# Kernel optimization log

Measured on AMD Instinct MI355X. Metric: run time of the kernel, lower is better.

Reference implementation:

```python
import jax, jax.numpy as jnp
import numpy as np
import math

DIM = 1024
N_HEADS = 16
HEAD_DIM = DIM // N_HEADS  # 64
B, S = 2, 2048


def apply_rope(x, cos, sin):
    # x: [b, s, h, d]; cos/sin: [s, d//2]
    xr = x[..., 0::2]
    xi = x[..., 1::2]
    cos = cos[None, :, None, :]
    sin = sin[None, :, None, :]
    out_r = xr * cos - xi * sin
    out_i = xr * sin + xi * cos
    # interleave back: stack pairs on last axis then flatten
    return jnp.stack([out_r, out_i], axis=-1).reshape(x.shape)


def setup_inputs() -> dict:
    key = jax.random.key(0)
    ks = jax.random.split(key, 8)
    scale = 1.0 / math.sqrt(DIM)
    x = jax.random.normal(ks[0], (B, S, DIM), dtype=jnp.float32)
    attn_mask = jnp.zeros((1, 1, S, S), dtype=jnp.float32)
    pos = jnp.arange(S, dtype=jnp.float32)[:, None]
    inv_freq = 1.0 / (10000.0 ** (jnp.arange(0, HEAD_DIM, 2, dtype=jnp.float32) / HEAD_DIM))
    ang = pos * inv_freq[None, :]  # [S, HEAD_DIM//2]
    freqs_cos = jnp.cos(ang)
    freqs_sin = jnp.sin(ang)
    wq_w = jax.random.normal(ks[1], (DIM, DIM), dtype=jnp.float32) * scale
    wk_w = jax.random.normal(ks[2], (DIM, DIM), dtype=jnp.float32) * scale
    wv_w = jax.random.normal(ks[3], (DIM, DIM), dtype=jnp.float32) * scale
    wo_w = jax.random.normal(ks[4], (DIM, DIM), dtype=jnp.float32) * scale
    wq_b = jnp.zeros((DIM,), dtype=jnp.float32)
    wk_b = jnp.zeros((DIM,), dtype=jnp.float32)
    wv_b = jnp.zeros((DIM,), dtype=jnp.float32)
    return {"x": x, "attn_mask": attn_mask, "freqs_cos": freqs_cos,
            "freqs_sin": freqs_sin, "wq_w": wq_w, "wq_b": wq_b,
            "wk_w": wk_w, "wk_b": wk_b, "wv_w": wv_w, "wv_b": wv_b,
            "wo_w": wo_w}


def reference(x, attn_mask, freqs_cos, freqs_sin, wq_w, wq_b, wk_w, wk_b,
              wv_w, wv_b, wo_w):
    b, s, _ = x.shape
    xq = (x @ wq_w + wq_b).reshape(b, s, N_HEADS, HEAD_DIM)
    xk = (x @ wk_w + wk_b).reshape(b, s, N_HEADS, HEAD_DIM)
    xv = (x @ wv_w + wv_b).reshape(b, s, N_HEADS, HEAD_DIM)
    xq = apply_rope(xq, freqs_cos, freqs_sin)
    xk = apply_rope(xk, freqs_cos, freqs_sin)
    # scores: [b, h, sq, skv]
    scores = jnp.einsum('bqhd,bkhd->bhqk', xq, xk) / math.sqrt(HEAD_DIM)
    scores = scores + attn_mask
    probs = jax.nn.softmax(scores, axis=-1)
    out = jnp.einsum('bhqk,bkhd->bqhd', probs, xv).reshape(b, s, DIM)
    return out @ wo_w
```

## Files before the change

### kernel.cpp

```cpp
#include <hip/hip_runtime.h>
#include <math.h>
#include <stdint.h>

#define DIM   1024
#define NH    16
#define HD    64
#define BATCH 2
#define SEQ   2048
#define ROWS  (BATCH*SEQ)

typedef __attribute__((ext_vector_type(8))) short short8;
typedef __attribute__((ext_vector_type(4))) float f32x4;

__device__ __forceinline__ unsigned short f2bf(float f) {
    union { float f; unsigned u; } x; x.f = f;
    unsigned r = x.u + 0x7FFFu + ((x.u >> 16) & 1u);
    return (unsigned short)(r >> 16);
}
__device__ __forceinline__ float bf2f(unsigned short h) {
    union { unsigned u; float f; } x; x.u = ((unsigned)h) << 16;
    return x.f;
}

#define MFMA(a,b,c) __builtin_amdgcn_mfma_f32_16x16x32_bf16((a),(b),(c),0,0,0)

__device__ __forceinline__ void gl_lds16(const void* g, void* l) {
    __builtin_amdgcn_global_load_lds(
        (const __attribute__((address_space(1))) unsigned int*)g,
        (__attribute__((address_space(3))) unsigned int*)l,
        16, 0, 0);
}

__global__ __launch_bounds__(256) void splitx_kernel(
    const float* __restrict__ x, unsigned short* __restrict__ xh, unsigned short* __restrict__ xl)
{
    const size_t i = ((size_t)blockIdx.x * 256 + threadIdx.x) * 4;
    const float4 v = *(const float4*)&x[i];
    ushort4 h, l;
    h.x = f2bf(v.x); l.x = f2bf(v.x - bf2f(h.x));
    h.y = f2bf(v.y); l.y = f2bf(v.y - bf2f(h.y));
    h.z = f2bf(v.z); l.z = f2bf(v.z - bf2f(h.z));
    h.w = f2bf(v.w); l.w = f2bf(v.w - bf2f(h.w));
    *(ushort4*)&xh[i] = h;
    *(ushort4*)&xl[i] = l;
}

__global__ __launch_bounds__(256) void splitw_kernel(
    const float* __restrict__ w0, const float* __restrict__ w1,
    const float* __restrict__ w2, const float* __restrict__ w3,
    unsigned short* __restrict__ wth, unsigned short* __restrict__ wtl)
{
    __shared__ float tile[64][68];
    const int z = blockIdx.z;
    const float* W = (z == 0) ? w0 : (z == 1) ? w1 : (z == 2) ? w2 : w3;
    unsigned short* th = wth + (size_t)z * DIM * DIM;
    unsigned short* tl = wtl + (size_t)z * DIM * DIM;
    const int k0 = blockIdx.y * 64, n0 = blockIdx.x * 64;
    const int tr = threadIdx.x >> 4, tc = (threadIdx.x & 15) * 4;
    #pragma unroll
    for (int p = 0; p < 4; ++p) {
        const float4 v = *(const float4*)&W[(size_t)(k0 + tr + p*16) * DIM + n0 + tc];
        *(float4*)&tile[tr + p*16][tc] = v;
    }
    __syncthreads();
    #pragma unroll
    for (int p = 0; p < 4; ++p) {
        const int n = tr + p*16;
        ushort4 hv, lv;
        float v0 = tile[tc+0][n], v1 = tile[tc+1][n], v2 = tile[tc+2][n], v3 = tile[tc+3][n];
        hv.x = f2bf(v0); lv.x = f2bf(v0 - bf2f(hv.x));
        hv.y = f2bf(v1); lv.y = f2bf(v1 - bf2f(hv.y));
        hv.z = f2bf(v2); lv.z = f2bf(v2 - bf2f(hv.z));
        hv.w = f2bf(v3); lv.w = f2bf(v3 - bf2f(hv.w));
        *(ushort4*)&th[(size_t)(n0 + n) * DIM + k0 + tc] = hv;
        *(ushort4*)&tl[(size_t)(n0 + n) * DIM + k0 + tc] = lv;
    }
}

template<int MODE>
__global__ __launch_bounds__(256, 2) void gemm3_kernel(
    const unsigned short* __restrict__ Ah, const unsigned short* __restrict__ Al,
    const unsigned short* __restrict__ Wh0, const unsigned short* __restrict__ Wl0,
    const unsigned short* __restrict__ Wh1, const unsigned short* __restrict__ Wl1,
    const unsigned short* __restrict__ Wh2, const unsigned short* __restrict__ Wl2,
    const float* __restrict__ b0, const float* __restrict__ b1, const float* __restrict__ b2,
    const float* __restrict__ fc, const float* __restrict__ fs,
    unsigned short* __restrict__ q_h, unsigned short* __restrict__ q_l,
    unsigned short* __restrict__ k_h, unsigned short* __restrict__ k_l,
    unsigned short* __restrict__ vt_h, unsigned short* __restrict__ vt_l,
    float* __restrict__ outf)
{
    __shared__ __align__(16) unsigned short lah[128*32], lal[128*32];
    __shared__ __align__(16) unsigned short lbh[128*32], lbl[128*32];

    const int tid = threadIdx.x;
    const int lane = tid & 63;
    const int lx = lane & 15, lg = lane >> 4;
    const int wv = tid >> 6, wm = wv >> 1, wn = wv & 1;
    const int n0 = blockIdx.x * 128, m0 = blockIdx.y * 128;
    const int z = (MODE == 0) ? blockIdx.z : 3;

    const unsigned short *Wh, *Wl;
    const float* bias;
    if (MODE == 0) {
        Wh = (z == 0) ? Wh0 : (z == 1) ? Wh1 : Wh2;
        Wl = (z == 0) ? Wl0 : (z == 1) ? Wl1 : Wl2;
        bias = (z == 0) ? b0 : (z == 1) ? b1 : b2;
    } else { Wh = Wh0; Wl = Wl0; bias = nullptr; }

    const int sr  = tid >> 2;
    const int scb = (tid & 3) << 4;

    f32x4 acc[4][4] = {};
    uint4 ra0, ra1, rl0, rl1, rb0, rb1, rb2, rb3;

    auto loadA = [&](int k0i) {
        const size_t a0 = ((size_t)(m0 + sr)      * DIM + k0i) * 2 + scb;
        const size_t a1 = ((size_t)(m0 + sr + 64) * DIM + k0i) * 2 + scb;
        ra0 = *(const uint4*)((const char*)Ah + a0);
        ra1 = *(const uint4*)((const char*)Ah + a1);
        rl0 = *(const uint4*)((const char*)Al + a0);
        rl1 = *(const uint4*)((const char*)Al + a1);
        const size_t bb0 = ((size_t)(n0 + sr)      * DIM + k0i) * 2 + scb;
        const size_t bb1 = ((size_t)(n0 + sr + 64) * DIM + k0i) * 2 + scb;
        rb0 = *(const uint4*)((const char*)Wh + bb0);
        rb1 = *(const uint4*)((const char*)Wh + bb1);
        rb2 = *(const uint4*)((const char*)Wl + bb0);
        rb3 = *(const uint4*)((const char*)Wl + bb1);
    };

    loadA(0);
    for (int k0i = 0; k0i < DIM; k0i += 32) {
        __syncthreads();
        {
            const int o0 = sr*64 + scb, o1 = (sr + 64)*64 + scb;
            *(uint4*)((char*)lah + o0) = ra0; *(uint4*)((char*)lah + o1) = ra1;
            *(uint4*)((char*)lal + o0) = rl0; *(uint4*)((char*)lal + o1) = rl1;
            *(uint4*)((char*)lbh + o0) = rb0; *(uint4*)((char*)lbh + o1) = rb1;
            *(uint4*)((char*)lbl + o0) = rb2; *(uint4*)((char*)lbl + o1) = rb3;
        }
        __syncthreads();
        if (k0i + 32 < DIM) loadA(k0i + 32);

        short8 afh[4], afl[4], bfh[4], bfl[4];
        #pragma unroll
        for (int i = 0; i < 4; ++i) {
            const int ar = wm*64 + i*16 + lx;
            afh[i] = *(const short8*)((const char*)lah + ar*64 + lg*16);
            afl[i] = *(const short8*)((const char*)lal + ar*64 + lg*16);
            const int br = wn*64 + i*16 + lx;
            bfh[i] = *(const short8*)((const char*)lbh + br*64 + lg*16);
            bfl[i] = *(const short8*)((const char*)lbl + br*64 + lg*16);
        }
        #pragma unroll
        for (int i = 0; i < 4; ++i)
        #pragma unroll
        for (int jn = 0; jn < 4; ++jn) {
            acc[i][jn] = MFMA(afh[i], bfh[jn], acc[i][jn]);
            acc[i][jn] = MFMA(afh[i], bfl[jn], acc[i][jn]);
            acc[i][jn] = MFMA(afl[i], bfh[jn], acc[i][jn]);
        }
    }

    #pragma unroll
    for (int i = 0; i < 4; ++i) {
        const int tokbase = m0 + wm*64 + i*16 + lg*4;
        #pragma unroll
        for (int jn = 0; jn < 4; ++jn) {
            const int c = n0 + wn*64 + jn*16 + lx;
            float bv = (MODE == 0) ? bias[c] : 0.f;
            float vj[4];
            #pragma unroll
            for (int j = 0; j < 4; ++j) vj[j] = acc[i][jn][j] + bv;
            if (MODE == 0 && z < 2) {
                const int i0 = (c & 63) >> 1;
                #pragma unroll
                for (int j = 0; j < 4; ++j) {
                    const int s = (tokbase + j) & (SEQ - 1);
                    const float cv = fc[s*32 + i0], sv = fs[s*32 + i0];
                    const float pv = __shfl_xor(vj[j], 1);
                    vj[j] = (c & 1) ? (pv*sv + vj[j]*cv) : (vj[j]*cv - pv*sv);
                }
            }
            if (MODE == 1) {
                #pragma unroll
                for (int j = 0; j < 4; ++j)
                    outf[(size_t)(tokbase + j) * DIM + c] = vj[j];
            } else if (z < 2) {
                unsigned short* oh = z ? k_h : q_h;
                unsigned short* ol = z ? k_l : q_l;
                #pragma unroll
                for (int j = 0; j < 4; ++j) {
                    const unsigned short hi = f2bf(vj[j]);
                    oh[(size_t)(tokbase + j) * DIM + c] = hi;
                    ol[(size_t)(tokbase + j) * DIM + c] = f2bf(vj[j] - bf2f(hi));
                }
            } else {
                const int bb = tokbase >> 11, s0 = tokbase & (SEQ - 1);
                const int hh = c >> 6, d = c & 63;
                const size_t vb = ((size_t)(bb*NH + hh) * HD + d) * SEQ + s0;
                ushort4 hv, lv;
                #pragma unroll
                for (int j = 0; j < 4; ++j) {
                    const unsigned short hi = f2bf(vj[j]);
                    ((unsigned short*)&hv)[j] = hi;
                    ((unsigned short*)&lv)[j] = f2bf(vj[j] - bf2f(hi));
                }
                *(ushort4*)&vt_h[vb] = hv;
                *(ushort4*)&vt_l[vb] = lv;
            }
        }
    }
}

__global__ __launch_bounds__(256, 2) void attn_kernel(
    const unsigned short* __restrict__ Qh, const unsigned short* __restrict__ Ql,
    const unsigned short* __restrict__ Kh, const unsigned short* __restrict__ Kl,
    const unsigned short* __restrict__ Vth, const unsigned short* __restrict__ Vtl,
    const float* __restrict__ mask,
    unsigned short* __restrict__ AOh, unsigned short* __restrict__ AOl)
{
    __shared__ __align__(16) unsigned short kbh[2][64*64], kbl[2][64*64];
    __shared__ __align__(16) unsigned short vbh[2][64*64], vbl[2][64*64];
    __shared__ __align__(16) unsigned short pb[4][2][16*32];

    const int tid = threadIdx.x;
    const int w = tid >> 6, lane = tid & 63;
    const int lx = lane & 15, lg = lane >> 4;
    const int qblk = blockIdx.x * 128;
    const int h = blockIdx.y, b = blockIdx.z;

    const int qrow0 = qblk + w*32 + lx;
    const int qrow1 = qrow0 + 16;

    short8 qf[2][2][2];
    {
        const size_t base0 = ((size_t)b*SEQ + qrow0) * DIM + h*HD + lg*8;
        const size_t base1 = ((size_t)b*SEQ + qrow1) * DIM + h*HD + lg*8;
        qf[0][0][0] = *(const short8*)&Qh[base0];  qf[0][0][1] = *(const short8*)&Qh[base0 + 32];
        qf[0][1][0] = *(const short8*)&Ql[base0];  qf[0][1][1] = *(const short8*)&Ql[base0 + 32];
        qf[1][0][0] = *(const short8*)&Qh[base1];  qf[1][0][1] = *(const short8*)&Qh[base1 + 32];
        qf[1][1][0] = *(const short8*)&Ql[base1];  qf[1][1][1] = *(const short8*)&Ql[base1 + 32];
    }

    float m_st[2] = {-INFINITY, -INFINITY}, l_st[2] = {0.f, 0.f};
    f32x4 acc[2][4] = {};

    const int sr  = tid >> 3;
    const int gco = ((tid & 7) * 16) ^ ((sr & 7) << 4);
    const int ldso = tid * 16;

    const char* khs = (const char*)Kh + ((size_t)b*SEQ + sr) * DIM * 2 + h*128 + gco;
    const char* kls = (const char*)Kl + ((size_t)b*SEQ + sr) * DIM * 2 + h*128 + gco;
    const char* vhs = (const char*)Vth + ((size_t)(b*NH + h)*HD + sr) * SEQ * 2 + gco;
    const char* vls = (const char*)Vtl + ((size_t)(b*NH + h)*HD + sr) * SEQ * 2 + gco;
    const size_t krs = (size_t)32 * DIM * 2;
    const size_t vrs = (size_t)32 * SEQ * 2;

    auto STAGE = [&](int t, int buf) {
        const size_t ko = (size_t)t * 64 * DIM * 2;
        const size_t vo = (size_t)t * 128;
        gl_lds16(khs + ko,       (char*)&kbh[buf][0] + ldso);
        gl_lds16(khs + ko + krs, (char*)&kbh[buf][0] + ldso + 4096);
        gl_lds16(kls + ko,       (char*)&kbl[buf][0] + ldso);
        gl_lds16(kls + ko + krs, (char*)&kbl[buf][0] + ldso + 4096);
        gl_lds16(vhs + vo,       (char*)&vbh[buf][0] + ldso);
        gl_lds16(vhs + vo + vrs, (char*)&vbh[buf][0] + ldso + 4096);
        gl_lds16(vls + vo,       (char*)&vbl[buf][0] + ldso);
        gl_lds16(vls + vo + vrs, (char*)&vbl[buf][0] + ldso + 4096);
    };

    STAGE(0, 0);
    __syncthreads();

    const float* mrow0 = mask + (size_t)qrow0 * SEQ;
    const float* mrow1 = mask + (size_t)qrow1 * SEQ;

    for (int t = 0; t < SEQ/64; ++t) {
        const int cur = t & 1;
        if (t + 1 < SEQ/64) STAGE(t + 1, cur ^ 1);

        float4 mk[2][4];
        #pragma unroll
        for (int mf = 0; mf < 4; ++mf) {
            mk[0][mf] = *(const float4*)&mrow0[t*64 + mf*16 + lg*4];
            mk[1][mf] = *(const float4*)&mrow1[t*64 + mf*16 + lg*4];
        }

        f32x4 st[2][4] = {};
        __builtin_amdgcn_s_setprio(1);
        #pragma unroll
        for (int ks = 0; ks < 2; ++ks) {
            #pragma unroll
            for (int mf = 0; mf < 4; ++mf) {
                const int row = mf*16 + lx;
                const int off = row*128 + ((ks*64 + lg*16) ^ ((row & 7) << 4));
                const short8 akh = *(const short8*)((const char*)&kbh[cur][0] + off);
                const short8 akl = *(const short8*)((const char*)&kbl[cur][0] + off);
                #pragma unroll
                for (int f = 0; f < 2; ++f) {
                    st[f][mf] = MFMA(akh, qf[f][0][ks], st[f][mf]);
                    st[f][mf] = MFMA(akh, qf[f][1][ks], st[f][mf]);
                    st[f][mf] = MFMA(akl, qf[f][0][ks], st[f][mf]);
                }
            }
        }
        __builtin_amdgcn_s_setprio(0);

        unsigned pw[2][4][2];
        #pragma unroll
        for (int f = 0; f < 2; ++f) {
            float p[4][4];
            float mx = -INFINITY;
            #pragma unroll
            for (int mf = 0; mf < 4; ++mf) {
                p[mf][0] = st[f][mf][0]*0.125f + mk[f][mf].x;
                p[mf][1] = st[f][mf][1]*0.125f + mk[f][mf].y;
                p[mf][2] = st[f][mf][2]*0.125f + mk[f][mf].z;
                p[mf][3] = st[f][mf][3]*0.125f + mk[f][mf].w;
                mx = fmaxf(mx, fmaxf(fmaxf(p[mf][0], p[mf][1]), fmaxf(p[mf][2], p[mf][3])));
            }
            mx = fmaxf(mx, __shfl_xor(mx, 16));
            mx = fmaxf(mx, __shfl_xor(mx, 32));
            const float mnew = fmaxf(m_st[f], mx);
            const float scl = __expf(m_st[f] - mnew);
            m_st[f] = mnew;

            float ps = 0.f;
            #pragma unroll
            for (int mf = 0; mf < 4; ++mf) {
                const float e0 = __expf(p[mf][0] - mnew), e1 = __expf(p[mf][1] - mnew);
                const float e2 = __expf(p[mf][2] - mnew), e3 = __expf(p[mf][3] - mnew);
                ps += (e0 + e1) + (e2 + e3);
                pw[f][mf][0] = (unsigned)f2bf(e0) | ((unsigned)f2bf(e1) << 16);
                pw[f][mf][1] = (unsigned)f2bf(e2) | ((unsigned)f2bf(e3) << 16);
            }
            ps += __shfl_xor(ps, 16);
            ps += __shfl_xor(ps, 32);
            l_st[f] = l_st[f]*scl + ps;

            float fj[4];
            #pragma unroll
            for (int j = 0; j < 4; ++j) fj[j] = __shfl(scl, lg*4 + j);
            #pragma unroll
            for (int nf = 0; nf < 4; ++nf)
                #pragma unroll
                for (int j = 0; j < 4; ++j) acc[f][nf][j] *= fj[j];
        }

        #pragma unroll
        for (int ks = 0; ks < 2; ++ks) {
            #pragma unroll
            for (int f = 0; f < 2; ++f)
                #pragma unroll
                for (int mm = 0; mm < 2; ++mm) {
                    const int off = lx*64 + ((mm*32 + lg*8) ^ ((lx & 3) << 4));
                    *(uint2*)((char*)&pb[w][f][0] + off) =
                        make_uint2(pw[f][ks*2 + mm][0], pw[f][ks*2 + mm][1]);
                }
            short8 pa[2];
            #pragma unroll
            for (int f = 0; f < 2; ++f) {
                const int poff = lx*64 + ((lg*16) ^ ((lx & 3) << 4));
                pa[f] = *(const short8*)((const char*)&pb[w][f][0] + poff);
            }
            __builtin_amdgcn_s_setprio(1);
            #pragma unroll
            for (int nf = 0; nf < 4; ++nf) {
                const int row = nf*16 + lx;
                const int off = row*128 + ((ks*64 + lg*16) ^ ((row & 7) << 4));
                const short8 vh = *(const short8*)((const char*)&vbh[cur][0] + off);
                const short8 vl = *(const short8*)((const char*)&vbl[cur][0] + off);
                #pragma unroll
                for (int f = 0; f < 2; ++f) {
                    acc[f][nf] = MFMA(pa[f], vh, acc[f][nf]);
                    acc[f][nf] = MFMA(pa[f], vl, acc[f][nf]);
                }
            }
            __builtin_amdgcn_s_setprio(0);
        }

        __syncthreads();
    }

    #pragma unroll
    for (int f = 0; f < 2; ++f) {
        float linv[4];
        #pragma unroll
        for (int j = 0; j < 4; ++j) linv[j] = 1.0f / __shfl(l_st[f], lg*4 + j);
        #pragma unroll
        for (int nf = 0; nf < 4; ++nf) {
            const int c = h*HD + nf*16 + lx;
            #pragma unroll
            for (int j = 0; j < 4; ++j) {
                const size_t tok = (size_t)b*SEQ + qblk + w*32 + f*16 + lg*4 + j;
                const float o = acc[f][nf][j] * linv[j];
                const unsigned short hi = f2bf(o);
                AOh[tok*DIM + c] = hi;
                AOl[tok*DIM + c] = f2bf(o - bf2f(hi));
            }
        }
    }
}

extern "C" void kernel_launch(void* const* d_in, const int* in_sizes, int n_in,
                              void* d_out, int out_size, void* d_ws, size_t ws_size,
                              hipStream_t stream)
{
    const float* x    = (const float*)d_in[0];
    const float* mask = (const float*)d_in[1];
    const float* fc   = (const float*)d_in[2];
    const float* fs   = (const float*)d_in[3];
    const float* wq   = (const float*)d_in[4];
    const float* bq   = (const float*)d_in[5];
    const float* wk   = (const float*)d_in[6];
    const float* bk   = (const float*)d_in[7];
    const float* wv   = (const float*)d_in[8];
    const float* bv   = (const float*)d_in[9];
    const float* wo   = (const float*)d_in[10];
    float* out = (float*)d_out;

    const size_t MB = 1024*1024;
    char* ws = (char*)d_ws;
    unsigned short* Xh  = (unsigned short*)(ws + 0*MB);
    unsigned short* Xl  = (unsigned short*)(ws + 8*MB);
    unsigned short* WTh = (unsigned short*)(ws + 16*MB);
    unsigned short* WTl = (unsigned short*)(ws + 24*MB);
    unsigned short* Qh  = (unsigned short*)(ws + 32*MB);
    unsigned short* Ql  = (unsigned short*)(ws + 40*MB);
    unsigned short* Kh  = (unsigned short*)(ws + 48*MB);
    unsigned short* Kl  = (unsigned short*)(ws + 56*MB);
    unsigned short* Vth = (unsigned short*)(ws + 64*MB);
    unsigned short* Vtl = (unsigned short*)(ws + 72*MB);
    unsigned short* AOh = Xh;
    unsigned short* AOl = Xl;

    const size_t WP = (size_t)DIM * DIM;

    splitx_kernel<<<(ROWS*DIM)/4/256, 256, 0, stream>>>(x, Xh, Xl);
    splitw_kernel<<<dim3(16, 16, 4), 256, 0, stream>>>(wq, wk, wv, wo, WTh, WTl);

    gemm3_kernel<0><<<dim3(8, 32, 3), 256, 0, stream>>>(
        Xh, Xl,
        WTh, WTl, WTh + WP, WTl + WP, WTh + 2*WP, WTl + 2*WP,
        bq, bk, bv, fc, fs,
        Qh, Ql, Kh, Kl, Vth, Vtl, nullptr);

    attn_kernel<<<dim3(SEQ/128, NH, BATCH), 256, 0, stream>>>(
        Qh, Ql, Kh, Kl, Vth, Vtl, mask, AOh, AOl);

    gemm3_kernel<1><<<dim3(8, 32, 1), 256, 0, stream>>>(
        AOh, AOl,
        WTh + 3*WP, WTl + 3*WP, nullptr, nullptr, nullptr, nullptr,
        nullptr, nullptr, nullptr, fc, fs,
        nullptr, nullptr, nullptr, nullptr, nullptr, nullptr, out);
    (void)in_sizes; (void)n_in; (void)out_size; (void)ws_size;
}
```

Measured before the change: 355.5 us.

## Switch split-precision MFMA from bf16 to fp16 and drop low-part operands

```diff
diff --git a/kernel.cpp b/kernel.cpp
--- a/kernel.cpp
+++ b/kernel.cpp
@@ -1,4 +1,5 @@
 #include <hip/hip_runtime.h>
+#include <hip/hip_fp16.h>
 #include <math.h>
 #include <stdint.h>
 
@@ -12,17 +13,16 @@
 typedef __attribute__((ext_vector_type(8))) short short8;
 typedef __attribute__((ext_vector_type(4))) float f32x4;
 
-__device__ __forceinline__ unsigned short f2bf(float f) {
-    union { float f; unsigned u; } x; x.f = f;
-    unsigned r = x.u + 0x7FFFu + ((x.u >> 16) & 1u);
-    return (unsigned short)(r >> 16);
-}
-__device__ __forceinline__ float bf2f(unsigned short h) {
-    union { unsigned u; float f; } x; x.u = ((unsigned)h) << 16;
-    return x.f;
-}
-
-#define MFMA(a,b,c) __builtin_amdgcn_mfma_f32_16x16x32_bf16((a),(b),(c),0,0,0)
+__device__ __forceinline__ unsigned short f2h(float f) {
+    __half h = __float2half(f);
+    return *(unsigned short*)&h;
+}
+__device__ __forceinline__ float h2f(unsigned short u) {
+    __half h = *(__half*)&u;
+    return __half2float(h);
+}
+
+#define MFMA16(a,b,c) __builtin_amdgcn_mfma_f32_16x16x32_f16((a),(b),(c),0,0,0)
 
 __device__ __forceinline__ void gl_lds16(const void* g, void* l) {
     __builtin_amdgcn_global_load_lds(
@@ -37,10 +37,10 @@
     const size_t i = ((size_t)blockIdx.x * 256 + threadIdx.x) * 4;
     const float4 v = *(const float4*)&x[i];
     ushort4 h, l;
-    h.x = f2bf(v.x); l.x = f2bf(v.x - bf2f(h.x));
-    h.y = f2bf(v.y); l.y = f2bf(v.y - bf2f(h.y));
-    h.z = f2bf(v.z); l.z = f2bf(v.z - bf2f(h.z));
-    h.w = f2bf(v.w); l.w = f2bf(v.w - bf2f(h.w));
+    h.x = f2h(v.x); l.x = f2h(v.x - h2f(h.x));
+    h.y = f2h(v.y); l.y = f2h(v.y - h2f(h.y));
+    h.z = f2h(v.z); l.z = f2h(v.z - h2f(h.z));
+    h.w = f2h(v.w); l.w = f2h(v.w - h2f(h.w));
     *(ushort4*)&xh[i] = h;
     *(ushort4*)&xl[i] = l;
 }
@@ -48,13 +48,12 @@
 __global__ __launch_bounds__(256) void splitw_kernel(
     const float* __restrict__ w0, const float* __restrict__ w1,
     const float* __restrict__ w2, const float* __restrict__ w3,
-    unsigned short* __restrict__ wth, unsigned short* __restrict__ wtl)
+    unsigned short* __restrict__ wt)
 {
     __shared__ float tile[64][68];
     const int z = blockIdx.z;
     const float* W = (z == 0) ? w0 : (z == 1) ? w1 : (z == 2) ? w2 : w3;
-    unsigned short* th = wth + (size_t)z * DIM * DIM;
-    unsigned short* tl = wtl + (size_t)z * DIM * DIM;
+    unsigned short* th = wt + (size_t)z * DIM * DIM;
     const int k0 = blockIdx.y * 64, n0 = blockIdx.x * 64;
     const int tr = threadIdx.x >> 4, tc = (threadIdx.x & 15) * 4;
     #pragma unroll
@@ -66,32 +65,27 @@
     #pragma unroll
     for (int p = 0; p < 4; ++p) {
         const int n = tr + p*16;
-        ushort4 hv, lv;
-        float v0 = tile[tc+0][n], v1 = tile[tc+1][n], v2 = tile[tc+2][n], v3 = tile[tc+3][n];
-        hv.x = f2bf(v0); lv.x = f2bf(v0 - bf2f(hv.x));
-        hv.y = f2bf(v1); lv.y = f2bf(v1 - bf2f(hv.y));
-        hv.z = f2bf(v2); lv.z = f2bf(v2 - bf2f(hv.z));
-        hv.w = f2bf(v3); lv.w = f2bf(v3 - bf2f(hv.w));
+        ushort4 hv;
+        hv.x = f2h(tile[tc+0][n]);
+        hv.y = f2h(tile[tc+1][n]);
+        hv.z = f2h(tile[tc+2][n]);
+        hv.w = f2h(tile[tc+3][n]);
         *(ushort4*)&th[(size_t)(n0 + n) * DIM + k0 + tc] = hv;
-        *(ushort4*)&tl[(size_t)(n0 + n) * DIM + k0 + tc] = lv;
     }
 }
 
 template<int MODE>
 __global__ __launch_bounds__(256, 2) void gemm3_kernel(
     const unsigned short* __restrict__ Ah, const unsigned short* __restrict__ Al,
-    const unsigned short* __restrict__ Wh0, const unsigned short* __restrict__ Wl0,
-    const unsigned short* __restrict__ Wh1, const unsigned short* __restrict__ Wl1,
-    const unsigned short* __restrict__ Wh2, const unsigned short* __restrict__ Wl2,
+    const unsigned short* __restrict__ W0, const unsigned short* __restrict__ W1,
+    const unsigned short* __restrict__ W2,
     const float* __restrict__ b0, const float* __restrict__ b1, const float* __restrict__ b2,
     const float* __restrict__ fc, const float* __restrict__ fs,
     unsigned short* __restrict__ q_h, unsigned short* __restrict__ q_l,
-    unsigned short* __restrict__ k_h, unsigned short* __restrict__ k_l,
-    unsigned short* __restrict__ vt_h, unsigned short* __restrict__ vt_l,
+    unsigned short* __restrict__ k_h, unsigned short* __restrict__ vt_h,
     float* __restrict__ outf)
 {
-    __shared__ __align__(16) unsigned short lah[128*32], lal[128*32];
-    __shared__ __align__(16) unsigned short lbh[128*32], lbl[128*32];
+    __shared__ __align__(16) unsigned short lah[128*32], lal[128*32], lbh[128*32];
 
     const int tid = threadIdx.x;
     const int lane = tid & 63;
@@ -100,19 +94,18 @@
     const int n0 = blockIdx.x * 128, m0 = blockIdx.y * 128;
     const int z = (MODE == 0) ? blockIdx.z : 3;
 
-    const unsigned short *Wh, *Wl;
+    const unsigned short* Wh;
     const float* bias;
     if (MODE == 0) {
-        Wh = (z == 0) ? Wh0 : (z == 1) ? Wh1 : Wh2;
-        Wl = (z == 0) ? Wl0 : (z == 1) ? Wl1 : Wl2;
+        Wh = (z == 0) ? W0 : (z == 1) ? W1 : W2;
         bias = (z == 0) ? b0 : (z == 1) ? b1 : b2;
-    } else { Wh = Wh0; Wl = Wl0; bias = nullptr; }
+    } else { Wh = W0; bias = nullptr; }
 
     const int sr  = tid >> 2;
     const int scb = (tid & 3) << 4;
 
     f32x4 acc[4][4] = {};
-    uint4 ra0, ra1, rl0, rl1, rb0, rb1, rb2, rb3;
+    uint4 ra0, ra1, rl0, rl1, rb0, rb1;
 
     auto loadA = [&](int k0i) {
         const size_t a0 = ((size_t)(m0 + sr)      * DIM + k0i) * 2 + scb;
@@ -125,8 +118,6 @@
         const size_t bb1 = ((size_t)(n0 + sr + 64) * DIM + k0i) * 2 + scb;
         rb0 = *(const uint4*)((const char*)Wh + bb0);
         rb1 = *(const uint4*)((const char*)Wh + bb1);
-        rb2 = *(const uint4*)((const char*)Wl + bb0);
-        rb3 = *(const uint4*)((const char*)Wl + bb1);
     };
 
     loadA(0);
@@ -137,12 +128,11 @@
             *(uint4*)((char*)lah + o0) = ra0; *(uint4*)((char*)lah + o1) = ra1;
             *(uint4*)((char*)lal + o0) = rl0; *(uint4*)((char*)lal + o1) = rl1;
             *(uint4*)((char*)lbh + o0) = rb0; *(uint4*)((char*)lbh + o1) = rb1;
-            *(uint4*)((char*)lbl + o0) = rb2; *(uint4*)((char*)lbl + o1) = rb3;
         }
         __syncthreads();
         if (k0i + 32 < DIM) loadA(k0i + 32);
 
-        short8 afh[4], afl[4], bfh[4], bfl[4];
+        short8 afh[4], afl[4], bfh[4];
         #pragma unroll
         for (int i = 0; i < 4; ++i) {
             const int ar = wm*64 + i*16 + lx;
@@ -150,15 +140,13 @@
             afl[i] = *(const short8*)((const char*)lal + ar*64 + lg*16);
             const int br = wn*64 + i*16 + lx;
             bfh[i] = *(const short8*)((const char*)lbh + br*64 + lg*16);
-            bfl[i] = *(const short8*)((const char*)lbl + br*64 + lg*16);
         }
         #pragma unroll
         for (int i = 0; i < 4; ++i)
         #pragma unroll
         for (int jn = 0; jn < 4; ++jn) {
-            acc[i][jn] = MFMA(afh[i], bfh[jn], acc[i][jn]);
-            acc[i][jn] = MFMA(afh[i], bfl[jn], acc[i][jn]);
-            acc[i][jn] = MFMA(afl[i], bfh[jn], acc[i][jn]);
+            acc[i][jn] = MFMA16(afh[i], bfh[jn], acc[i][jn]);
+            acc[i][jn] = MFMA16(afl[i], bfh[jn], acc[i][jn]);
         }
     }
 
@@ -186,48 +174,42 @@
                 #pragma unroll
                 for (int j = 0; j < 4; ++j)
                     outf[(size_t)(tokbase + j) * DIM + c] = vj[j];
-            } else if (z < 2) {
-                unsigned short* oh = z ? k_h : q_h;
-                unsigned short* ol = z ? k_l : q_l;
+            } else if (z == 0) {
                 #pragma unroll
                 for (int j = 0; j < 4; ++j) {
-                    const unsigned short hi = f2bf(vj[j]);
-                    oh[(size_t)(tokbase + j) * DIM + c] = hi;
-                    ol[(size_t)(tokbase + j) * DIM + c] = f2bf(vj[j] - bf2f(hi));
+                    const unsigned short hi = f2h(vj[j]);
+                    q_h[(size_t)(tokbase + j) * DIM + c] = hi;
+                    q_l[(size_t)(tokbase + j) * DIM + c] = f2h(vj[j] - h2f(hi));
                 }
+            } else if (z == 1) {
+                #pragma unroll
+                for (int j = 0; j < 4; ++j)
+                    k_h[(size_t)(tokbase + j) * DIM + c] = f2h(vj[j]);
             } else {
                 const int bb = tokbase >> 11, s0 = tokbase & (SEQ - 1);
                 const int hh = c >> 6, d = c & 63;
                 const size_t vb = ((size_t)(bb*NH + hh) * HD + d) * SEQ + s0;
-                ushort4 hv, lv;
-                #pragma unroll
-                for (int j = 0; j < 4; ++j) {
-                    const unsigned short hi = f2bf(vj[j]);
-                    ((unsigned short*)&hv)[j] = hi;
-                    ((unsigned short*)&lv)[j] = f2bf(vj[j] - bf2f(hi));
-                }
+                ushort4 hv;
+                hv.x = f2h(vj[0]); hv.y = f2h(vj[1]); hv.z = f2h(vj[2]); hv.w = f2h(vj[3]);
                 *(ushort4*)&vt_h[vb] = hv;
-                *(ushort4*)&vt_l[vb] = lv;
-            }
-        }
-    }
-}
-
-__global__ __launch_bounds__(256, 2) void attn_kernel(
+            }
+        }
+    }
+}
+
+__global__ __launch_bounds__(128, 2) void attn_kernel(
     const unsigned short* __restrict__ Qh, const unsigned short* __restrict__ Ql,
-    const unsigned short* __restrict__ Kh, const unsigned short* __restrict__ Kl,
-    const unsigned short* __restrict__ Vth, const unsigned short* __restrict__ Vtl,
+    const unsigned short* __restrict__ Kh, const unsigned short* __restrict__ Vth,
     const float* __restrict__ mask,
     unsigned short* __restrict__ AOh, unsigned short* __restrict__ AOl)
 {
-    __shared__ __align__(16) unsigned short kbh[2][64*64], kbl[2][64*64];
-    __shared__ __align__(16) unsigned short vbh[2][64*64], vbl[2][64*64];
-    __shared__ __align__(16) unsigned short pb[4][2][16*32];
+    __shared__ __align__(16) unsigned short kb[2][64*64], vb[2][64*64];
+    __shared__ __align__(16) unsigned short pb[2][2][16*32];
 
     const int tid = threadIdx.x;
     const int w = tid >> 6, lane = tid & 63;
     const int lx = lane & 15, lg = lane >> 4;
-    const int qblk = blockIdx.x * 128;
+    const int qblk = blockIdx.x * 64;
     const int h = blockIdx.y, b = blockIdx.z;
 
     const int qrow0 = qblk + w*32 + lx;
@@ -251,23 +233,18 @@
     const int ldso = tid * 16;
 
     const char* khs = (const char*)Kh + ((size_t)b*SEQ + sr) * DIM * 2 + h*128 + gco;
-    const char* kls = (const char*)Kl + ((size_t)b*SEQ + sr) * DIM * 2 + h*128 + gco;
     const char* vhs = (const char*)Vth + ((size_t)(b*NH + h)*HD + sr) * SEQ * 2 + gco;
-    const char* vls = (const char*)Vtl + ((size_t)(b*NH + h)*HD + sr) * SEQ * 2 + gco;
-    const size_t krs = (size_t)32 * DIM * 2;
-    const size_t vrs = (size_t)32 * SEQ * 2;
+    const size_t krs = (size_t)16 * DIM * 2;
+    const size_t vrs = (size_t)16 * SEQ * 2;
 
     auto STAGE = [&](int t, int buf) {
         const size_t ko = (size_t)t * 64 * DIM * 2;
         const size_t vo = (size_t)t * 128;
-        gl_lds16(khs + ko,       (char*)&kbh[buf][0] + ldso);
-        gl_lds16(khs + ko + krs, (char*)&kbh[buf][0] + ldso + 4096);
-        gl_lds16(kls + ko,       (char*)&kbl[buf][0] + ldso);
-        gl_lds16(kls + ko + krs, (char*)&kbl[buf][0] + ldso + 4096);
-        gl_lds16(vhs + vo,       (char*)&vbh[buf][0] + ldso);
-        gl_lds16(vhs + vo + vrs, (char*)&vbh[buf][0] + ldso + 4096);
-        gl_lds16(vls + vo,       (char*)&vbl[buf][0] + ldso);
-        gl_lds16(vls + vo + vrs, (char*)&vbl[buf][0] + ldso + 4096);
+        #pragma unroll
+        for (int s4 = 0; s4 < 4; ++s4) {
+            gl_lds16(khs + ko + s4*krs, (char*)&kb[buf][0] + ldso + s4*2048);
+            gl_lds16(vhs + vo + s4*vrs, (char*)&vb[buf][0] + ldso + s4*2048);
+        }
     };
 
     STAGE(0, 0);
@@ -295,13 +272,11 @@
             for (int mf = 0; mf < 4; ++mf) {
                 const int row = mf*16 + lx;
                 const int off = row*128 + ((ks*64 + lg*16) ^ ((row & 7) << 4));
-                const short8 akh = *(const short8*)((const char*)&kbh[cur][0] + off);
-                const short8 akl = *(const short8*)((const char*)&kbl[cur][0] + off);
+                const short8 akh = *(const short8*)((const char*)&kb[cur][0] + off);
                 #pragma unroll
                 for (int f = 0; f < 2; ++f) {
-                    st[f][mf] = MFMA(akh, qf[f][0][ks], st[f][mf]);
-                    st[f][mf] = MFMA(akh, qf[f][1][ks], st[f][mf]);
-                    st[f][mf] = MFMA(akl, qf[f][0][ks], st[f][mf]);
+                    st[f][mf] = MFMA16(akh, qf[f][0][ks], st[f][mf]);
+                    st[f][mf] = MFMA16(akh, qf[f][1][ks], st[f][mf]);
                 }
             }
         }
@@ -322,30 +297,33 @@
             }
             mx = fmaxf(mx, __shfl_xor(mx, 16));
             mx = fmaxf(mx, __shfl_xor(mx, 32));
-            const float mnew = fmaxf(m_st[f], mx);
-            const float scl = __expf(m_st[f] - mnew);
-            m_st[f] = mnew;
+
+            if (!__all(mx <= m_st[f] + 8.0f)) {
+                const float mnew = fmaxf(m_st[f], mx);
+                const float scl = __expf(m_st[f] - mnew);
+                m_st[f] = mnew;
+                l_st[f] *= scl;
+                float fj[4];
+                #pragma unroll
+                for (int j = 0; j < 4; ++j) fj[j] = __shfl(scl, lg*4 + j);
+                #pragma unroll
+                for (int nf = 0; nf < 4; ++nf)
+                    #pragma unroll
+                    for (int j = 0; j < 4; ++j) acc[f][nf][j] *= fj[j];
+            }
 
             float ps = 0.f;
             #pragma unroll
             for (int mf = 0; mf < 4; ++mf) {
-                const float e0 = __expf(p[mf][0] - mnew), e1 = __expf(p[mf][1] - mnew);
-                const float e2 = __expf(p[mf][2] - mnew), e3 = __expf(p[mf][3] - mnew);
+                const float e0 = __expf(p[mf][0] - m_st[f]), e1 = __expf(p[mf][1] - m_st[f]);
+                const float e2 = __expf(p[mf][2] - m_st[f]), e3 = __expf(p[mf][3] - m_st[f]);
                 ps += (e0 + e1) + (e2 + e3);
-                pw[f][mf][0] = (unsigned)f2bf(e0) | ((unsigned)f2bf(e1) << 16);
-                pw[f][mf][1] = (unsigned)f2bf(e2) | ((unsigned)f2bf(e3) << 16);
+                pw[f][mf][0] = (unsigned)f2h(e0) | ((unsigned)f2h(e1) << 16);
+                pw[f][mf][1] = (unsigned)f2h(e2) | ((unsigned)f2h(e3) << 16);
             }
             ps += __shfl_xor(ps, 16);
             ps += __shfl_xor(ps, 32);
-            l_st[f] = l_st[f]*scl + ps;
-
-            float fj[4];
-            #pragma unroll
-            for (int j = 0; j < 4; ++j) fj[j] = __shfl(scl, lg*4 + j);
-            #pragma unroll
-            for (int nf = 0; nf < 4; ++nf)
-                #pragma unroll
-                for (int j = 0; j < 4; ++j) acc[f][nf][j] *= fj[j];
+            l_st[f] += ps;
         }
 
         #pragma unroll
@@ -369,13 +347,10 @@
             for (int nf = 0; nf < 4; ++nf) {
                 const int row = nf*16 + lx;
                 const int off = row*128 + ((ks*64 + lg*16) ^ ((row & 7) << 4));
-                const short8 vh = *(const short8*)((const char*)&vbh[cur][0] + off);
-                const short8 vl = *(const short8*)((const char*)&vbl[cur][0] + off);
-                #pragma unroll
-                for (int f = 0; f < 2; ++f) {
-                    acc[f][nf] = MFMA(pa[f], vh, acc[f][nf]);
-                    acc[f][nf] = MFMA(pa[f], vl, acc[f][nf]);
-                }
+                const short8 vh = *(const short8*)((const char*)&vb[cur][0] + off);
+                #pragma unroll
+                for (int f = 0; f < 2; ++f)
+                    acc[f][nf] = MFMA16(pa[f], vh, acc[f][nf]);
             }
             __builtin_amdgcn_s_setprio(0);
         }
@@ -395,9 +370,9 @@
             for (int j = 0; j < 4; ++j) {
                 const size_t tok = (size_t)b*SEQ + qblk + w*32 + f*16 + lg*4 + j;
                 const float o = acc[f][nf][j] * linv[j];
-                const unsigned short hi = f2bf(o);
+                const unsigned short hi = f2h(o);
                 AOh[tok*DIM + c] = hi;
-                AOl[tok*DIM + c] = f2bf(o - bf2f(hi));
+                AOl[tok*DIM + c] = f2h(o - h2f(hi));
             }
         }
     }
@@ -424,35 +399,32 @@
     char* ws = (char*)d_ws;
     unsigned short* Xh  = (unsigned short*)(ws + 0*MB);
     unsigned short* Xl  = (unsigned short*)(ws + 8*MB);
-    unsigned short* WTh = (unsigned short*)(ws + 16*MB);
-    unsigned short* WTl = (unsigned short*)(ws + 24*MB);
-    unsigned short* Qh  = (unsigned short*)(ws + 32*MB);
-    unsigned short* Ql  = (unsigned short*)(ws + 40*MB);
-    unsigned short* Kh  = (unsigned short*)(ws + 48*MB);
-    unsigned short* Kl  = (unsigned short*)(ws + 56*MB);
-    unsigned short* Vth = (unsigned short*)(ws + 64*MB);
-    unsigned short* Vtl = (unsigned short*)(ws + 72*MB);
+    unsigned short* WT  = (unsigned short*)(ws + 16*MB);
+    unsigned short* Qh  = (unsigned short*)(ws + 24*MB);
+    unsigned short* Ql  = (unsigned short*)(ws + 32*MB);
+    unsigned short* Kh  = (unsigned short*)(ws + 40*MB);
+    unsigned short* Vth = (unsigned short*)(ws + 48*MB);
     unsigned short* AOh = Xh;
     unsigned short* AOl = Xl;
 
     const size_t WP = (size_t)DIM * DIM;
 
     splitx_kernel<<<(ROWS*DIM)/4/256, 256, 0, stream>>>(x, Xh, Xl);
-    splitw_kernel<<<dim3(16, 16, 4), 256, 0, stream>>>(wq, wk, wv, wo, WTh, WTl);
+    splitw_kernel<<<dim3(16, 16, 4), 256, 0, stream>>>(wq, wk, wv, wo, WT);
 
     gemm3_kernel<0><<<dim3(8, 32, 3), 256, 0, stream>>>(
         Xh, Xl,
-        WTh, WTl, WTh + WP, WTl + WP, WTh + 2*WP, WTl + 2*WP,
+        WT, WT + WP, WT + 2*WP,
         bq, bk, bv, fc, fs,
-        Qh, Ql, Kh, Kl, Vth, Vtl, nullptr);
-
-    attn_kernel<<<dim3(SEQ/128, NH, BATCH), 256, 0, stream>>>(
-        Qh, Ql, Kh, Kl, Vth, Vtl, mask, AOh, AOl);
+        Qh, Ql, Kh, Vth, nullptr);
+
+    attn_kernel<<<dim3(SEQ/64, NH, BATCH), 128, 0, stream>>>(
+        Qh, Ql, Kh, Vth, mask, AOh, AOl);
 
     gemm3_kernel<1><<<dim3(8, 32, 1), 256, 0, stream>>>(
         AOh, AOl,
-        WTh + 3*WP, WTl + 3*WP, nullptr, nullptr, nullptr, nullptr,
+        WT + 3*WP, nullptr, nullptr,
         nullptr, nullptr, nullptr, fc, fs,
-        nullptr, nullptr, nullptr, nullptr, nullptr, nullptr, out);
+        nullptr, nullptr, nullptr, nullptr, out);
     (void)in_sizes; (void)n_in; (void)out_size; (void)ws_size;
 }
```

New measurement: 304.3 us. 14.4% less time.
